# Kernel optimization log

Measured on AMD Instinct MI355X. Metric: run time of the kernel, lower is better.

Reference implementation:

```python
import jax, jax.numpy as jnp
import numpy as np

IN_C = 256
GROUPS = 32
ED = 256  # ResnetBlock embed_dim
EPS = 1e-5
B, L = 16, 2048


def setup_inputs() -> dict:
    key = jax.random.key(0)
    ks = jax.random.split(key, 8)

    def rn(k, shape, s=0.05):
        return jax.random.normal(k, shape, dtype=jnp.float32) * s

    d = {
        "x": jax.random.normal(ks[0], (B, IN_C, L), dtype=jnp.float32),
        "t": jax.random.normal(ks[1], (B, 256, 1), dtype=jnp.float32),
    }
    i = 2
    for p in ["r1", "r2"]:
        d[f"{p}_gn1_w"] = jnp.ones((IN_C,), jnp.float32)
        d[f"{p}_gn1_b"] = jnp.zeros((IN_C,), jnp.float32)
        d[f"{p}_c1_w"] = rn(ks[i], (ED, IN_C, 3)); i += 1
        d[f"{p}_c1_b"] = jnp.zeros((ED,), jnp.float32)
        d[f"{p}_gn2_w"] = jnp.ones((ED,), jnp.float32)
        d[f"{p}_gn2_b"] = jnp.zeros((ED,), jnp.float32)
        d[f"{p}_c2_w"] = rn(ks[i], (IN_C, ED, 3)); i += 1
        d[f"{p}_c2_b"] = jnp.zeros((IN_C,), jnp.float32)
    d["lin_w"] = rn(ks[i], (3 * IN_C, IN_C, 1))
    d["lin_b"] = jnp.zeros((3 * IN_C,), jnp.float32)
    return d


def _gn(x, w, b):
    # GroupNorm over (C//G, L) per group, affine per-channel
    Bx, C, Lx = x.shape
    xr = x.reshape(Bx, GROUPS, -1)
    m = xr.mean(-1, keepdims=True)
    v = xr.var(-1, keepdims=True)
    xr = (xr - m) * jax.lax.rsqrt(v + EPS)
    return xr.reshape(Bx, C, Lx) * w[None, :, None] + b[None, :, None]


def _conv(x, w, b, pad):
    y = jax.lax.conv_general_dilated(
        x, w, window_strides=(1,), padding=[(pad, pad)],
        dimension_numbers=("NCH", "OIH", "NCH"))
    return y + b[None, :, None]


def _res(x, t, gn1w, gn1b, c1w, c1b, gn2w, gn2b, c2w, c2b):
    h = _conv(jax.nn.relu(_gn(x, gn1w, gn1b)), c1w, c1b, 1) + t
    h = _conv(jax.nn.relu(_gn(h, gn2w, gn2b)), c2w, c2b, 1)
    return x + h


def reference(x, t,
              r1_gn1_w, r1_gn1_b, r1_c1_w, r1_c1_b, r1_gn2_w, r1_gn2_b, r1_c2_w, r1_c2_b,
              r2_gn1_w, r2_gn1_b, r2_c1_w, r2_c1_b, r2_gn2_w, r2_gn2_b, r2_c2_w, r2_c2_b,
              lin_w, lin_b):
    x = _res(x, t, r1_gn1_w, r1_gn1_b, r1_c1_w, r1_c1_b, r1_gn2_w, r1_gn2_b, r1_c2_w, r1_c2_b)
    kqv = _conv(x, lin_w, lin_b, 0)                      # (B, 3C, L)
    kt, qt, vt = jnp.split(kqv, 3, axis=1)               # each (B, C, L)
    scale = 1.0 / np.sqrt(x.shape[1]).astype(np.float32)
    scores = jnp.einsum("bcq,bck->bqk", qt, kt) * scale  # (B, L, L)
    attn = jax.nn.softmax(scores, axis=2)
    av = jnp.einsum("bqk,bck->bcq", attn, vt)            # (B, C, L)
    return _res(av, t, r2_gn1_w, r2_gn1_b, r2_c1_w, r2_c1_b, r2_gn2_w, r2_gn2_b, r2_c2_w, r2_c2_b)
```

## Files before the change

### kernel.cpp

```cpp
#include <hip/hip_runtime.h>

typedef unsigned short u16;
typedef unsigned int u32;
typedef __attribute__((ext_vector_type(8))) short bf16x8;
typedef __attribute__((ext_vector_type(4))) float f32x4;
typedef __attribute__((ext_vector_type(16))) float f32x16;

#define NB 16
#define NC 256
#define NL 2048
#define EPS 1e-5f
#define QSC2 0.0901684401f
#define DEFER 11.54f
#define TROWS 2050
#define PHALF ((size_t)NB * NC * NL)

__device__ __forceinline__ float bf2f(u16 a) {
  union { unsigned u; float f; } v; v.u = (unsigned)a << 16; return v.f;
}
__device__ __forceinline__ u16 f2bf(float f) {
  union { float f; unsigned u; } v; v.f = f;
  return (u16)((v.u + 0x7fffu + ((v.u >> 16) & 1u)) >> 16);
}
__device__ __forceinline__ u32 cvtpk(float lo, float hi) {
  u32 r;
  asm("v_cvt_pk_bf16_f32 %0, %1, %2" : "=v"(r) : "v"(lo), "v"(hi));
  return r;
}
__device__ __forceinline__ float ex2(float x) {
  float r;
  asm("v_exp_f32 %0, %1" : "=v"(r) : "v"(x));
  return r;
}
__device__ __forceinline__ void gld16(const void* gsrc, void* ldst) {
  __builtin_amdgcn_global_load_lds(
      (const __attribute__((address_space(1))) void*)gsrc,
      (__attribute__((address_space(3))) void*)ldst, 16, 0, 0);
}

__global__ __launch_bounds__(256)
void pack_w(const float* __restrict__ w1, const float* __restrict__ w2,
            const float* __restrict__ w3, const float* __restrict__ w4,
            const float* __restrict__ lw, const float* __restrict__ lb,
            u16* __restrict__ Wp, u16* __restrict__ Wq, float* __restrict__ bq)
{
  const int a = blockIdx.y;
  const int gid = blockIdx.x * 256 + threadIdx.x;
  if (a < 4) {
    const float* w = a == 0 ? w1 : a == 1 ? w2 : a == 2 ? w3 : w4;
    const int d = gid >> 16, rem = gid & 65535;
    const int oc = rem >> 8, ic = rem & 255;
    Wp[a * 196608 + gid] = f2bf(w[(oc * 256 + ic) * 3 + d]);
  } else {
    const int oc = gid >> 8;
    const float s = (oc >= 256 && oc < 512) ? QSC2 : 1.0f;
    Wq[gid] = f2bf(lw[gid] * s);
    if (gid < 768) bq[gid] = lb[gid] * ((gid >= 256 && gid < 512) ? QSC2 : 1.0f);
  }
}

__global__ __launch_bounds__(256)
void stats_f32(const float* __restrict__ x, float2* __restrict__ pstat)
{
  const int blk = blockIdx.x;
  const float* p = x + (size_t)blk * NL + threadIdx.x * 8;
  const float4 a = ((const float4*)p)[0];
  const float4 c4 = ((const float4*)p)[1];
  float s = (a.x + a.y) + (a.z + a.w) + (c4.x + c4.y) + (c4.z + c4.w);
  float ss = a.x*a.x + a.y*a.y + a.z*a.z + a.w*a.w + c4.x*c4.x + c4.y*c4.y + c4.z*c4.z + c4.w*c4.w;
#pragma unroll
  for (int o = 32; o > 0; o >>= 1) { s += __shfl_down(s, o); ss += __shfl_down(ss, o); }
  __shared__ float2 red[4];
  if ((threadIdx.x & 63) == 0) red[threadIdx.x >> 6] = make_float2(s, ss);
  __syncthreads();
  if (threadIdx.x == 0)
    pstat[blk] = make_float2(red[0].x + red[1].x + red[2].x + red[3].x,
                             red[0].y + red[1].y + red[2].y + red[3].y);
}

__global__ __launch_bounds__(256)
void apply_f32T(const float* __restrict__ x, const float2* __restrict__ pstat,
                const float* __restrict__ gw, const float* __restrict__ gb,
                u16* __restrict__ outT)
{
  __shared__ float2 chs[256];
  __shared__ float gm[32], gi[32];
  __shared__ float ta[32][257];
  const int t = threadIdx.x, b = blockIdx.y;
  const int L0 = blockIdx.x * 32;
  chs[t] = pstat[b * 256 + t];
  __syncthreads();
  if (t < 32) {
    float S = 0.f, SS = 0.f;
#pragma unroll
    for (int j = 0; j < 8; ++j) { S += chs[t * 8 + j].x; SS += chs[t * 8 + j].y; }
    const float mean = S * (1.f / 16384.f);
    const float var = SS * (1.f / 16384.f) - mean * mean;
    gm[t] = mean; gi[t] = rsqrtf(var + EPS);
  }
  {
    const int cR = t >> 3, lq = (t & 7) * 4;
#pragma unroll
    for (int i = 0; i < 8; ++i) {
      const int c = i * 32 + cR;
      const float4 v = *(const float4*)&x[((size_t)b * NC + c) * NL + L0 + lq];
      ta[lq + 0][c] = v.x; ta[lq + 1][c] = v.y; ta[lq + 2][c] = v.z; ta[lq + 3][c] = v.w;
    }
  }
  __syncthreads();
  const int g = t & 31, rbase = t >> 5;
  float ga[8], be[8];
#pragma unroll
  for (int j = 0; j < 4; ++j)
#pragma unroll
    for (int k = 0; k < 2; ++k) {
      const int c = 2 * g + 64 * j + k;
      const int grp = c >> 3;
      ga[j * 2 + k] = gw[c] * gi[grp];
      be[j * 2 + k] = gb[c] - gm[grp] * ga[j * 2 + k];
    }
#pragma unroll
  for (int ri = 0; ri < 4; ++ri) {
    const int row = rbase + ri * 8;
    u16* orow = outT + ((size_t)b * TROWS + 1 + L0 + row) * 256;
#pragma unroll
    for (int j = 0; j < 4; ++j) {
      const int c = 2 * g + 64 * j;
      const float v0 = ta[row][c], v1 = ta[row][c + 1];
      ushort2 o;
      o.x = f2bf(fmaxf(fmaf(v0, ga[j * 2], be[j * 2]), 0.f));
      o.y = f2bf(fmaxf(fmaf(v1, ga[j * 2 + 1], be[j * 2 + 1]), 0.f));
      *(ushort2*)(orow + c) = o;
    }
  }
  if (blockIdx.x == 0 && t < 128) {
    const int r = (t >> 6) ? 2049 : 0;
    *(ushort4*)(outT + ((size_t)b * TROWS + r) * 256 + (t & 63) * 4) = (ushort4){0, 0, 0, 0};
  }
}

__global__ __launch_bounds__(256)
void apply_TT(const u16* __restrict__ inT, const float2* __restrict__ pstat,
              const float* __restrict__ gw, const float* __restrict__ gb,
              u16* __restrict__ outT)
{
  __shared__ float2 chs[256];
  __shared__ float gm[32], gi[32];
  const int t = threadIdx.x, b = blockIdx.y;
  {
    float S = 0.f, SS = 0.f;
#pragma unroll
    for (int p = 0; p < 16; ++p) {
      const float2 v = pstat[((size_t)b * 16 + p) * 256 + t];
      S += v.x; SS += v.y;
    }
    chs[t] = make_float2(S, SS);
  }
  __syncthreads();
  if (t < 32) {
    float S = 0.f, SS = 0.f;
#pragma unroll
    for (int j = 0; j < 8; ++j) { S += chs[t * 8 + j].x; SS += chs[t * 8 + j].y; }
    const float mean = S * (1.f / 16384.f);
    const float var = SS * (1.f / 16384.f) - mean * mean;
    gm[t] = mean; gi[t] = rsqrtf(var + EPS);
  }
  __syncthreads();
  const int g = t & 31;
  float ga[8], be[8];
#pragma unroll
  for (int j = 0; j < 8; ++j) {
    ga[j] = gw[g * 8 + j] * gi[g];
    be[j] = gb[g * 8 + j] - gm[g] * ga[j];
  }
#pragma unroll
  for (int j = 0; j < 16; ++j) {
    const int row = blockIdx.x * 128 + j * 8 + (t >> 5);
    const size_t off = ((size_t)b * TROWS + 1 + row) * 256 + g * 8;
    const bf16x8 h = *(const bf16x8*)(inT + off);
    u16 o[8];
#pragma unroll
    for (int i = 0; i < 8; ++i)
      o[i] = f2bf(fmaxf(fmaf(bf2f(((const u16*)&h)[i]), ga[i], be[i]), 0.f));
    *(bf16x8*)(outT + off) = *(bf16x8*)o;
  }
  if (blockIdx.x == 0 && t < 128) {
    const int r = (t >> 6) ? 2049 : 0;
    *(ushort4*)(outT + ((size_t)b * TROWS + r) * 256 + (t & 63) * 4) = (ushort4){0, 0, 0, 0};
  }
}

template<int OCT, int KD, bool HAS_T, int RESM, bool STATS>
__global__ __launch_bounds__(256, 2)
void conv_mfma(const u16* __restrict__ xT, const u16* __restrict__ Wp,
               const float* __restrict__ bias, const float* __restrict__ tadd,
               u16* __restrict__ outT, u16* __restrict__ vTout,
               const float* __restrict__ resf, const u16* __restrict__ resT,
               float* __restrict__ outf, float2* __restrict__ pstatOut)
{
  constexpr int DOFF = (KD == 3) ? 0 : 1;
  __shared__ __align__(16) u16 xs[2][130 * 128];
  const int bx = blockIdx.x;
  const int b = blockIdx.z;
  int lbx, ocb0, nsub;
  if (OCT == 256) {
    const int wid = (bx & 7) * 4 + (bx >> 3);
    lbx = wid >> 1; ocb0 = (wid & 1) * 128; nsub = 1;
  } else {
    const int wid = (bx & 7) * 8 + (bx >> 3);
    const int yy = wid & 3;
    lbx = wid >> 2;
    if (yy < 2) { ocb0 = yy * 256; nsub = 2; }
    else { ocb0 = 512 + (yy - 2) * 128; nsub = 1; }
  }
  const int lb = lbx * 128;
  const int tid = threadIdx.x;
  const int w = tid >> 6, lane = tid & 63;
  const int l15 = lane & 15, lg = lane >> 4;
  const int woc = (w >> 1) * 64, wl = (w & 1) * 64;

  const u16* xTb = xT + ((size_t)b * TROWS + lb) * 256;

  auto stageX = [&](int buf, int ich) {
    u16* xb = &xs[buf][0];
#pragma unroll
    for (int j = 0; j < 8; ++j) {
      const int slot = w * 512 + j * 64 + lane;
      const int row = slot >> 4, g0 = slot & 15;
      const int g = (g0 & 8) | ((g0 ^ row) & 7);
      gld16(xTb + (size_t)row * 256 + ich * 128 + g * 8, xb + (size_t)(w * 512 + j * 64) * 8);
    }
    if (w == 0 && lane < 32) {
      const int slot = 2048 + lane;
      const int row = slot >> 4, g0 = slot & 15;
      const int g = (g0 & 8) | ((g0 ^ row) & 7);
      gld16(xTb + (size_t)row * 256 + ich * 128 + g * 8, xb + (size_t)2048 * 8);
    }
  };
  auto loadW = [&](bf16x8 (&af)[KD][4], int p, int ocb) {
    const int ich = p >> 2, kc = p & 3;
#pragma unroll
    for (int d = 0; d < KD; ++d)
#pragma unroll
      for (int mf = 0; mf < 4; ++mf)
        af[d][mf] = *(const bf16x8*)(Wp + ((size_t)d * OCT + ocb + woc + mf * 16 + l15) * 256
                                        + ich * 128 + kc * 32 + lg * 8);
  };

  stageX(0, 0);
  __syncthreads();
  stageX(1, 1);

  for (int sidx = 0; sidx < nsub; ++sidx) {
    const int ocb = ocb0 + sidx * 128;
    f32x4 acc[4][4];
#pragma unroll
    for (int i = 0; i < 4; ++i)
#pragma unroll
      for (int j = 0; j < 4; ++j) acc[i][j] = (f32x4){0.f, 0.f, 0.f, 0.f};

    bf16x8 afbuf[2][KD][4];
    loadW(afbuf[0], 0, ocb);

#pragma unroll
    for (int p = 0; p < 8; ++p) {
      if (p == 4 && sidx == 0) __syncthreads();
      if (p < 7) loadW(afbuf[(p + 1) & 1], p + 1, ocb);
      const int kc = p & 3;
      const int gg = kc * 4 + lg;
      const char* xb = (const char*)&xs[p >> 2][0];
#pragma unroll
      for (int nf = 0; nf < 4; ++nf) {
#pragma unroll
        for (int d = 0; d < KD; ++d) {
          const int r = wl + nf * 16 + l15 + d + DOFF;
          const int gsr = (gg & 8) | ((gg ^ r) & 7);
          const bf16x8 bf = *(const bf16x8*)(xb + r * 256 + gsr * 16);
#pragma unroll
          for (int mf = 0; mf < 4; ++mf)
            acc[mf][nf] = __builtin_amdgcn_mfma_f32_16x16x32_bf16(afbuf[p & 1][d][mf], bf, acc[mf][nf], 0, 0, 0);
        }
      }
    }

    if (OCT == 768 && ocb0 >= 512) {
      __syncthreads();
      u16* tile = (u16*)&xs[0][0];
#pragma unroll
      for (int mf = 0; mf < 4; ++mf) {
        const int cl = woc + mf * 16 + lg * 4;
        const float4 bv = *(const float4*)&bias[ocb + cl];
#pragma unroll
        for (int nf = 0; nf < 4; ++nf) {
          const int ll = wl + nf * 16 + l15;
          const f32x4 a = acc[mf][nf];
          tile[(cl + 0) * 136 + ll] = f2bf(a[0] + bv.x);
          tile[(cl + 1) * 136 + ll] = f2bf(a[1] + bv.y);
          tile[(cl + 2) * 136 + ll] = f2bf(a[2] + bv.z);
          tile[(cl + 3) * 136 + ll] = f2bf(a[3] + bv.w);
        }
      }
      __syncthreads();
      const int cv0 = ocb - 512;
#pragma unroll
      for (int it = 0; it < 8; ++it) {
        const int chunk = it * 256 + tid;
        const int row = chunk >> 4, off = (chunk & 15) * 8;
        const bf16x8 v = *(const bf16x8*)&tile[row * 136 + off];
        *(bf16x8*)(vTout + ((size_t)b * NC + cv0 + row) * NL + lb + off) = v;
      }
      return;
    }

    float cs[4][4], cq[4][4];
    if (STATS) {
#pragma unroll
      for (int i = 0; i < 4; ++i)
#pragma unroll
        for (int j = 0; j < 4; ++j) { cs[i][j] = 0.f; cq[i][j] = 0.f; }
    }

#pragma unroll
    for (int mf = 0; mf < 4; ++mf) {
      const int ocbase = ocb + woc + mf * 16 + lg * 4;
      float4 bv = *(const float4*)&bias[ocbase];
      if (HAS_T) {
        const float4 tv = *(const float4*)&tadd[b * 256 + ocbase];
        bv.x += tv.x; bv.y += tv.y; bv.z += tv.z; bv.w += tv.w;
      }
#pragma unroll
      for (int nf = 0; nf < 4; ++nf) {
        const int l = lb + wl + nf * 16 + l15;
        const f32x4 a = acc[mf][nf];
        float v0 = a[0] + bv.x, v1 = a[1] + bv.y, v2 = a[2] + bv.z, v3 = a[3] + bv.w;
        if (RESM == 1) {
          const float* rp = resf + ((size_t)b * NC + ocbase) * NL + l;
          v0 += rp[0]; v1 += rp[NL]; v2 += rp[2 * (size_t)NL]; v3 += rp[3 * (size_t)NL];
        }
        if (RESM == 2) {
          const ushort4 rv = *(const ushort4*)(resT + ((size_t)b * TROWS + 1 + l) * 256 + ocbase);
          v0 += bf2f(rv.x); v1 += bf2f(rv.y); v2 += bf2f(rv.z); v3 += bf2f(rv.w);
        }
        if (STATS) {
          cs[mf][0] += v0; cq[mf][0] += v0 * v0;
          cs[mf][1] += v1; cq[mf][1] += v1 * v1;
          cs[mf][2] += v2; cq[mf][2] += v2 * v2;
          cs[mf][3] += v3; cq[mf][3] += v3 * v3;
        }
        if (RESM == 2) {
          float* op = outf + ((size_t)b * NC + ocbase) * NL + l;
          op[0] = v0; op[NL] = v1; op[2 * (size_t)NL] = v2; op[3 * (size_t)NL] = v3;
        } else if (OCT == 256) {
          ushort4 st = {f2bf(v0), f2bf(v1), f2bf(v2), f2bf(v3)};
          *(ushort4*)(outT + ((size_t)b * TROWS + 1 + l) * 256 + ocbase) = st;
        } else {
          ushort4 st = {f2bf(v0), f2bf(v1), f2bf(v2), f2bf(v3)};
          *(ushort4*)(outT + ((size_t)b * NL + l) * 512 + ocbase) = st;
        }
      }
    }

    if (STATS) {
      __syncthreads();
      float* sred = (float*)&xs[0][0];
#pragma unroll
      for (int mf = 0; mf < 4; ++mf)
#pragma unroll
        for (int j = 0; j < 4; ++j) {
          float s = cs[mf][j], q = cq[mf][j];
#pragma unroll
          for (int m = 1; m < 16; m <<= 1) { s += __shfl_xor(s, m); q += __shfl_xor(q, m); }
          if (l15 == 0) {
            const int cl = woc + mf * 16 + lg * 4 + j;
            sred[(w & 1) * 128 + cl] = s;
            sred[256 + (w & 1) * 128 + cl] = q;
          }
        }
      __syncthreads();
      if (tid < 128) {
        const float s = sred[tid] + sred[128 + tid];
        const float q = sred[256 + tid] + sred[384 + tid];
        pstatOut[((size_t)b * 16 + lbx) * 256 + ocb + tid] = make_float2(s, q);
      }
    }
  }
}

#define AKVB 32
#define ATILES 32

__global__ __launch_bounds__(256, 2)
void attn_mfma(const u16* __restrict__ kq, const u16* __restrict__ vT,
               u16* __restrict__ part, float2* __restrict__ stats)
{
  __shared__ u16 ks[2][32 * 256];
  __shared__ u16 vs[2][256 * 32];

  const int fid = blockIdx.x;
  const int xcd = fid & 7, idx = fid >> 3;
  const int b = (xcd << 1) | (idx & 1);
  const int rest = idx >> 1;
  const int qt = rest & 15, half = rest >> 4;
  const int kvbase = half * 1024;

  const int tid = threadIdx.x;
  const int w = tid >> 6, lane = tid & 63;
  const int l31 = lane & 31, lh = lane >> 5;
  const int q = qt * 128 + w * 32 + l31;

  const u16* kqb = kq + (size_t)b * NL * 512;
  const u16* vb  = vT + (size_t)b * NC * NL;

  auto stage = [&](int buf, int kv0) {
#pragma unroll
    for (int j = 0; j < 4; ++j) {
      const int slot = w * 256 + j * 64 + lane;
      const int r = slot >> 5, c = slot & 31;
      const int g = (c - r) & 31;
      gld16(kqb + (size_t)(kv0 + r) * 512 + g * 8, &ks[buf][(size_t)(w * 256 + j * 64) * 8]);
    }
#pragma unroll
    for (int j = 0; j < 4; ++j) {
      const int slot = w * 256 + j * 64 + lane;
      const int r = slot >> 2, c = slot & 3;
      const int g = (c - r - (r >> 2)) & 3;
      gld16(vb + (size_t)r * NL + kv0 + g * 8, &vs[buf][(size_t)(w * 256 + j * 64) * 8]);
    }
  };

  bf16x8 qf[16];
  {
    const u16* qp = kqb + (size_t)q * 512 + 256 + lh * 8;
#pragma unroll
    for (int kk = 0; kk < 16; ++kk) qf[kk] = *(const bf16x8*)(qp + kk * 16);
  }

  f32x16 o[8];
#pragma unroll
  for (int i = 0; i < 8; ++i)
    o[i] = (f32x16){0.f,0.f,0.f,0.f,0.f,0.f,0.f,0.f,0.f,0.f,0.f,0.f,0.f,0.f,0.f,0.f};
  float m = -1e30f, lsum = 0.f;

  stage(0, kvbase);
  __syncthreads();

  for (int t = 0; t < ATILES; ++t) {
    const int cur = t & 1;
    if (t + 1 < ATILES) stage(cur ^ 1, kvbase + (t + 1) * AKVB);
    const u16* kbase = &ks[cur][0];
    f32x16 s = (f32x16){0.f,0.f,0.f,0.f,0.f,0.f,0.f,0.f,0.f,0.f,0.f,0.f,0.f,0.f,0.f,0.f};
#pragma unroll
    for (int kk = 0; kk < 16; ++kk) {
      const int gn = 2 * kk + lh;
      const bf16x8 kf = *(const bf16x8*)(kbase + (l31 * 32 + ((gn + l31) & 31)) * 8);
      s = __builtin_amdgcn_mfma_f32_32x32x16_bf16(kf, qf[kk], s, 0, 0, 0);
    }
    float tm = s[0];
#pragma unroll
    for (int i = 1; i < 16; ++i) tm = fmaxf(tm, s[i]);
    tm = fmaxf(tm, __shfl_xor(tm, 32));
    if (!__all(tm <= m + DEFER)) {
      const float mn = fmaxf(m, tm);
      const float corr = ex2(m - mn);
      m = mn; lsum *= corr;
#pragma unroll
      for (int i = 0; i < 8; ++i) o[i] *= corr;
    }
    float sum = 0.f;
#pragma unroll
    for (int i = 0; i < 16; ++i) { s[i] = ex2(s[i] - m); sum += s[i]; }
    sum += __shfl_xor(sum, 32);
    lsum += sum;
    u32 pk[8];
#pragma unroll
    for (int i = 0; i < 8; ++i) pk[i] = cvtpk(s[2 * i], s[2 * i + 1]);
    const u16* vbase = &vs[cur][0];
#pragma unroll
    for (int ksx = 0; ksx < 2; ++ksx) {
      const int base = ksx * 4;
      const u32 send0 = lh ? pk[base + 0] : pk[base + 2];
      const u32 send1 = lh ? pk[base + 1] : pk[base + 3];
      const u32 r0 = (u32)__shfl_xor((int)send0, 32);
      const u32 r1 = (u32)__shfl_xor((int)send1, 32);
      union { u32 wd[4]; bf16x8 v; } pu;
      pu.wd[0] = lh ? r0 : pk[base + 0];
      pu.wd[1] = lh ? r1 : pk[base + 1];
      pu.wd[2] = lh ? pk[base + 2] : r0;
      pu.wd[3] = lh ? pk[base + 3] : r1;
      const bf16x8 pf = pu.v;
      const int gn = 2 * ksx + lh;
#pragma unroll
      for (int mf = 0; mf < 8; ++mf) {
        const int row = mf * 32 + l31;
        const bf16x8 vf = *(const bf16x8*)(vbase + (row * 4 + ((gn + row + (row >> 2)) & 3)) * 8);
        o[mf] = __builtin_amdgcn_mfma_f32_32x32x16_bf16(vf, pf, o[mf], 0, 0, 0);
      }
    }
    if (t + 1 < ATILES) __syncthreads();
  }
  u16* pp = part + half * PHALF + (size_t)b * NC * NL + q;
#pragma unroll
  for (int mf = 0; mf < 8; ++mf)
#pragma unroll
    for (int r = 0; r < 16; ++r) {
      const int c = mf * 32 + (r & 3) + 8 * (r >> 2) + 4 * lh;
      pp[(size_t)c * NL] = f2bf(o[mf][r]);
    }
  if (lane < 32)
    stats[((size_t)half * NB + b) * NL + q] = make_float2(m, lsum);
}

__global__ __launch_bounds__(256)
void attn_combine(const u16* __restrict__ part, const float2* __restrict__ stats,
                  u16* __restrict__ avT, float2* __restrict__ pstat)
{
  __shared__ float2 sst[2][128];
  __shared__ u16 tile[128][264];
  const int chunk = blockIdx.x, b = blockIdx.y;
  const int t = threadIdx.x;
  const int l0 = chunk * 128;
  if (t < 128) sst[0][t] = stats[(size_t)b * NL + l0 + t];
  else sst[1][t - 128] = stats[((size_t)NB + b) * NL + l0 + (t - 128)];
  __syncthreads();
  const u16* p0 = part + ((size_t)b * NC + t) * NL + l0;
  const u16* p1 = p0 + PHALF;
  float s = 0.f, ss = 0.f;
#pragma unroll 4
  for (int j = 0; j < 16; ++j) {
    const bf16x8 a8 = *(const bf16x8*)(p0 + j * 8);
    const bf16x8 b8 = *(const bf16x8*)(p1 + j * 8);
#pragma unroll
    for (int k = 0; k < 8; ++k) {
      const int l = j * 8 + k;
      const float2 sa = sst[0][l], sb = sst[1][l];
      const float M = fmaxf(sa.x, sb.x);
      const float e0 = ex2(sa.x - M), e1 = ex2(sb.x - M);
      const float den = 1.f / (sa.y * e0 + sb.y * e1);
      const float r = (bf2f(((const u16*)&a8)[k]) * e0 + bf2f(((const u16*)&b8)[k]) * e1) * den;
      tile[l][t] = f2bf(r);
      s += r; ss += r * r;
    }
  }
  pstat[((size_t)b * 16 + chunk) * 256 + t] = make_float2(s, ss);
  __syncthreads();
#pragma unroll
  for (int it = 0; it < 16; ++it) {
    const int id = it * 256 + t;
    const int row = id >> 5, ch = id & 31;
    const bf16x8 v = *(const bf16x8*)&tile[row][ch * 8];
    *(bf16x8*)(avT + ((size_t)b * TROWS + 1 + l0 + row) * 256 + ch * 8) = v;
  }
}

extern "C" void kernel_launch(void* const* d_in, const int* in_sizes, int n_in,
                              void* d_out, int out_size, void* d_ws, size_t ws_size,
                              hipStream_t stream)
{
  (void)in_sizes; (void)n_in; (void)out_size; (void)ws_size;
  const float* x        = (const float*)d_in[0];
  const float* t        = (const float*)d_in[1];
  const float* r1_gn1_w = (const float*)d_in[2];
  const float* r1_gn1_b = (const float*)d_in[3];
  const float* r1_c1_w  = (const float*)d_in[4];
  const float* r1_c1_b  = (const float*)d_in[5];
  const float* r1_gn2_w = (const float*)d_in[6];
  const float* r1_gn2_b = (const float*)d_in[7];
  const float* r1_c2_w  = (const float*)d_in[8];
  const float* r1_c2_b  = (const float*)d_in[9];
  const float* r2_gn1_w = (const float*)d_in[10];
  const float* r2_gn1_b = (const float*)d_in[11];
  const float* r2_c1_w  = (const float*)d_in[12];
  const float* r2_c1_b  = (const float*)d_in[13];
  const float* r2_gn2_w = (const float*)d_in[14];
  const float* r2_gn2_b = (const float*)d_in[15];
  const float* r2_c2_w  = (const float*)d_in[16];
  const float* r2_c2_b  = (const float*)d_in[17];
  const float* lin_w    = (const float*)d_in[18];
  const float* lin_b    = (const float*)d_in[19];

  float* out = (float*)d_out;

  const size_t TSZ = (size_t)NB * TROWS * 256 * 2;
  u16* tA  = (u16*)d_ws;
  u16* tB  = (u16*)((char*)d_ws + TSZ);
  u16* kq  = tB;
  u16* tC  = (u16*)((char*)d_ws + 3 * TSZ);
  u16* vT  = tC;
  u16* Wp  = (u16*)((char*)d_ws + 4 * TSZ);
  u16* Wq  = Wp + 4 * 196608;
  float* bq = (float*)(Wq + 196608);
  float2* pstat = (float2*)((char*)bq + 4096);
  float2* astat = (float2*)((char*)pstat + 524288);

  const dim3 gPack(768, 5);
  const dim3 gC(32, 1, NB);
  const dim3 gQ(64, 1, NB);
  const dim3 gS16(16, NB);
  const dim3 gA64(64, NB);
  const dim3 gCmb(16, NB);

  pack_w<<<gPack, 256, 0, stream>>>(r1_c1_w, r1_c2_w, r2_c1_w, r2_c2_w, lin_w, lin_b, Wp, Wq, bq);

  stats_f32<<<NB * NC, 256, 0, stream>>>(x, pstat);
  apply_f32T<<<gA64, 256, 0, stream>>>(x, pstat, r1_gn1_w, r1_gn1_b, tA);
  conv_mfma<256, 3, true, 0, true><<<gC, 256, 0, stream>>>(tA, Wp, r1_c1_b, t, tB, nullptr, nullptr, nullptr, nullptr, pstat);
  apply_TT<<<gS16, 256, 0, stream>>>(tB, pstat, r1_gn2_w, r1_gn2_b, tC);
  conv_mfma<256, 3, false, 1, false><<<gC, 256, 0, stream>>>(tC, Wp + 196608, r1_c2_b, nullptr, tA, nullptr, x, nullptr, nullptr, nullptr);

  conv_mfma<768, 1, false, 0, false><<<gQ, 256, 0, stream>>>(tA, Wq, bq, nullptr, kq, vT, nullptr, nullptr, nullptr, nullptr);
  attn_mfma<<<512, 256, 0, stream>>>(kq, vT, (u16*)out, astat);
  attn_combine<<<gCmb, 256, 0, stream>>>((const u16*)out, astat, tA, pstat);

  apply_TT<<<gS16, 256, 0, stream>>>(tA, pstat, r2_gn1_w, r2_gn1_b, tC);
  conv_mfma<256, 3, true, 0, true><<<gC, 256, 0, stream>>>(tC, Wp + 2 * 196608, r2_c1_b, t, tB, nullptr, nullptr, nullptr, nullptr, pstat);
  apply_TT<<<gS16, 256, 0, stream>>>(tB, pstat, r2_gn2_w, r2_gn2_b, tC);
  conv_mfma<256, 3, false, 2, false><<<gC, 256, 0, stream>>>(tC, Wp + 3 * 196608, r2_c2_b, nullptr, nullptr, nullptr, nullptr, tA, out, nullptr);
}
```

Before: 359.0 us.

## Store attention partials row-major by query to vectorize writes and simplify combine

The attention kernel now writes its bf16 partial outputs in (batch, query, channel) layout using 8-byte vector stores instead of scattered 2-byte stores strided by NL. The combine kernel reads those partials along contiguous channels, computes the softmax merge factors once per row, and writes avT directly without the LDS transpose tile. Per-channel sum and sum-of-squares are now reduced across row groups through shared memory. This is meant to cut uncoalesced global stores and LDS transpose traffic, at the cost of a small extra reduction step.

```diff
diff --git a/kernel.cpp b/kernel.cpp
--- a/kernel.cpp
+++ b/kernel.cpp
@@ -498,13 +498,17 @@
     }
     if (t + 1 < ATILES) __syncthreads();
   }
-  u16* pp = part + half * PHALF + (size_t)b * NC * NL + q;
+  u16* pp = part + half * PHALF + ((size_t)b * NL + q) * 256;
 #pragma unroll
   for (int mf = 0; mf < 8; ++mf)
 #pragma unroll
-    for (int r = 0; r < 16; ++r) {
-      const int c = mf * 32 + (r & 3) + 8 * (r >> 2) + 4 * lh;
-      pp[(size_t)c * NL] = f2bf(o[mf][r]);
+    for (int rq = 0; rq < 4; ++rq) {
+      ushort4 st;
+      st.x = f2bf(o[mf][rq * 4 + 0]);
+      st.y = f2bf(o[mf][rq * 4 + 1]);
+      st.z = f2bf(o[mf][rq * 4 + 2]);
+      st.w = f2bf(o[mf][rq * 4 + 3]);
+      *(ushort4*)(pp + mf * 32 + 8 * rq + 4 * lh) = st;
     }
   if (lane < 32)
     stats[((size_t)half * NB + b) * NL + q] = make_float2(m, lsum);
@@ -515,40 +519,45 @@
                   u16* __restrict__ avT, float2* __restrict__ pstat)
 {
   __shared__ float2 sst[2][128];
-  __shared__ u16 tile[128][264];
+  __shared__ float redS[8][256], redQ[8][256];
   const int chunk = blockIdx.x, b = blockIdx.y;
   const int t = threadIdx.x;
+  const int rg = t >> 5;
+  const int cg = (t & 31) * 8;
   const int l0 = chunk * 128;
   if (t < 128) sst[0][t] = stats[(size_t)b * NL + l0 + t];
   else sst[1][t - 128] = stats[((size_t)NB + b) * NL + l0 + (t - 128)];
   __syncthreads();
-  const u16* p0 = part + ((size_t)b * NC + t) * NL + l0;
-  const u16* p1 = p0 + PHALF;
-  float s = 0.f, ss = 0.f;
+  float cs[8], cq[8];
+#pragma unroll
+  for (int k = 0; k < 8; ++k) { cs[k] = 0.f; cq[k] = 0.f; }
 #pragma unroll 4
   for (int j = 0; j < 16; ++j) {
-    const bf16x8 a8 = *(const bf16x8*)(p0 + j * 8);
-    const bf16x8 b8 = *(const bf16x8*)(p1 + j * 8);
+    const int l = j * 8 + rg;
+    const float2 sa = sst[0][l], sb = sst[1][l];
+    const float M = fmaxf(sa.x, sb.x);
+    const float e0 = ex2(sa.x - M), e1 = ex2(sb.x - M);
+    const float den = 1.f / (sa.y * e0 + sb.y * e1);
+    const size_t off = ((size_t)b * NL + l0 + l) * 256 + cg;
+    const bf16x8 a8 = *(const bf16x8*)(part + off);
+    const bf16x8 b8 = *(const bf16x8*)(part + PHALF + off);
+    u16 o8[8];
 #pragma unroll
     for (int k = 0; k < 8; ++k) {
-      const int l = j * 8 + k;
-      const float2 sa = sst[0][l], sb = sst[1][l];
-      const float M = fmaxf(sa.x, sb.x);
-      const float e0 = ex2(sa.x - M), e1 = ex2(sb.x - M);
-      const float den = 1.f / (sa.y * e0 + sb.y * e1);
       const float r = (bf2f(((const u16*)&a8)[k]) * e0 + bf2f(((const u16*)&b8)[k]) * e1) * den;
-      tile[l][t] = f2bf(r);
-      s += r; ss += r * r;
-    }
-  }
-  pstat[((size_t)b * 16 + chunk) * 256 + t] = make_float2(s, ss);
-  __syncthreads();
-#pragma unroll
-  for (int it = 0; it < 16; ++it) {
-    const int id = it * 256 + t;
-    const int row = id >> 5, ch = id & 31;
-    const bf16x8 v = *(const bf16x8*)&tile[row][ch * 8];
-    *(bf16x8*)(avT + ((size_t)b * TROWS + 1 + l0 + row) * 256 + ch * 8) = v;
+      o8[k] = f2bf(r);
+      cs[k] += r; cq[k] += r * r;
+    }
+    *(bf16x8*)(avT + ((size_t)b * TROWS + 1 + l0 + l) * 256 + cg) = *(bf16x8*)o8;
+  }
+#pragma unroll
+  for (int k = 0; k < 8; ++k) { redS[rg][cg + k] = cs[k]; redQ[rg][cg + k] = cq[k]; }
+  __syncthreads();
+  {
+    float S = 0.f, Q = 0.f;
+#pragma unroll
+    for (int r = 0; r < 8; ++r) { S += redS[r][t]; Q += redQ[r][t]; }
+    pstat[((size_t)b * 16 + chunk) * 256 + t] = make_float2(S, Q);
   }
 }
 
```

New measurement: 346.5 us. 1.04x faster.
